# Performance work log

Hardware: AMD Instinct MI355X
Metric: run time of the kernel (lower is better)

Reference implementation:

```python
import jax, jax.numpy as jnp
import numpy as np
from jax import lax

B, S, D, H_HEADS, K, G, E, HID = 2, 1024, 1024, 16, 31, 4, 2, 2048
HD = D // H_HEADS

def _layer_norm(x, g, b, eps=1e-5):
    mu = jnp.mean(x, axis=-1, keepdims=True)
    var = jnp.mean(jnp.square(x - mu), axis=-1, keepdims=True)
    return (x - mu) * lax.rsqrt(var + eps) * g + b

def setup_inputs() -> dict:
    key = jax.random.key(0)
    ks = jax.random.split(key, 16)
    s = 0.02
    return {
        "x": jax.random.normal(ks[0], (B, S, D), jnp.float32),
        "group_ids": jax.random.randint(ks[1], (B, S), 0, G, jnp.int32),
        "cn_g": jnp.ones((D,), jnp.float32), "cn_b": jnp.zeros((D,), jnp.float32),
        "conv_w": jax.random.normal(ks[2], (D, D, K), jnp.float32) * s,
        "conv_b": jnp.zeros((D,), jnp.float32),
        "an_g": jnp.ones((D,), jnp.float32), "an_b": jnp.zeros((D,), jnp.float32),
        "in_w": jax.random.normal(ks[3], (3 * D, D), jnp.float32) * s,
        "in_b": jnp.zeros((3 * D,), jnp.float32),
        "out_w": jax.random.normal(ks[4], (D, D), jnp.float32) * s,
        "out_b": jnp.zeros((D,), jnp.float32),
        "e_w1": jax.random.normal(ks[5], (G, E, D, HID), jnp.float32) * s,
        "e_b1": jnp.zeros((G, E, HID), jnp.float32),
        "e_w2": jax.random.normal(ks[6], (G, E, HID, D), jnp.float32) * s,
        "e_b2": jnp.zeros((G, E, D), jnp.float32),
    }

def reference(x, group_ids, cn_g, cn_b, conv_w, conv_b, an_g, an_b,
              in_w, in_b, out_w, out_b, e_w1, e_b1, e_w2, e_b2):
    # ---- conv block (dropout off: deterministic/eval) ----
    residual = x
    h = _layer_norm(x, cn_g, cn_b)
    hc = jnp.transpose(h, (0, 2, 1))  # [B, D, S]
    hc = lax.conv_general_dilated(hc, conv_w, window_strides=(1,),
                                  padding=[(K // 2, K // 2)],
                                  dimension_numbers=("NCH", "OIH", "NCH"))
    hc = hc + conv_b[None, :, None]
    hc = jnp.transpose(hc, (0, 2, 1))
    x = jax.nn.gelu(hc, approximate=False) + residual
    # ---- self-attention block ----
    residual = x
    h = _layer_norm(x, an_g, an_b)
    qkv = h @ in_w.T + in_b  # [B, S, 3D]
    q, k, v = jnp.split(qkv, 3, axis=-1)
    q = q.reshape(B, S, H_HEADS, HD)
    k = k.reshape(B, S, H_HEADS, HD)
    v = v.reshape(B, S, H_HEADS, HD)
    scores = jnp.einsum("bqhd,bkhd->bhqk", q, k) / jnp.sqrt(jnp.float32(HD))
    attn = jax.nn.softmax(scores, axis=-1)
    ctx = jnp.einsum("bhqk,bkhd->bqhd", attn, v).reshape(B, S, D)
    x = ctx @ out_w.T + out_b + residual
    # ---- group-routed MoE (dense compute over groups, select by group id) ----
    residual = x
    xf = x.reshape(B * S, D)
    gid = group_ids.reshape(B * S)
    h1 = jax.nn.gelu(jnp.einsum("nd,gedh->ngeh", xf, e_w1) + e_b1, approximate=False)
    out_all = jnp.einsum("ngeh,gehd->nged", h1, e_w2) + e_b2  # [N, G, E, D]
    out_all = jnp.mean(out_all, axis=2)  # mean over experts in group -> [N, G, D]
    sel = jnp.take_along_axis(out_all, gid[:, None, None].astype(jnp.int32), axis=1)[:, 0]
    x = sel.reshape(B, S, D) + residual
    return x
```

## Files before the change

kernel.cpp:

```cpp
#include <hip/hip_runtime.h>
#include <hip/hip_bf16.h>
#include <math.h>

#define BB 2
#define SS 1024
#define DD 1024
#define HH 16
#define HDIM 64
#define KK 31
#define GG 4
#define EE 2
#define HIDN 2048
#define NTOK (BB*SS)
#define D3 (3*DD)

typedef unsigned short u16;
typedef __attribute__((ext_vector_type(8))) short s16x8;
typedef __attribute__((ext_vector_type(8))) unsigned short u16x8;
typedef __attribute__((ext_vector_type(4))) unsigned short u16x4;
typedef __attribute__((ext_vector_type(2))) unsigned short u16x2;
typedef __attribute__((ext_vector_type(4))) float f32x4;
typedef __attribute__((ext_vector_type(2))) unsigned int u32x2;

__device__ __forceinline__ float gelu_f(float x) {
  return 0.5f * x * (1.0f + erff(x * 0.7071067811865475f));
}
__device__ __forceinline__ u16 f2bf(float f) {
  unsigned u = __builtin_bit_cast(unsigned, f);
  u = (u + 0x7fffu + ((u >> 16) & 1u)) >> 16;
  return (u16)u;
}
__device__ __forceinline__ float bf2f(u16 u) {
  return __builtin_bit_cast(float, ((unsigned)u) << 16);
}
__device__ __forceinline__ f32x4 MFMA16(s16x8 a, s16x8 b, f32x4 c) {
  return __builtin_amdgcn_mfma_f32_16x16x32_bf16(a, b, c, 0, 0, 0);
}
#define GLOAD16(gp, lp) __builtin_amdgcn_global_load_lds( \
    (const __attribute__((address_space(1))) void*)(gp),  \
    (__attribute__((address_space(3))) void*)(lp), 16, 0, 0)

__global__ void ln_kernel(const float* __restrict__ x, const float* __restrict__ g,
                          const float* __restrict__ b, u16* __restrict__ out) {
  const int row = blockIdx.x;
  const int tid = threadIdx.x;
  __shared__ float red[4];
  const float4 v = reinterpret_cast<const float4*>(x + (size_t)row * DD)[tid];
  float s = v.x + v.y + v.z + v.w;
  s += __shfl_down(s, 32); s += __shfl_down(s, 16); s += __shfl_down(s, 8);
  s += __shfl_down(s, 4);  s += __shfl_down(s, 2);  s += __shfl_down(s, 1);
  if ((tid & 63) == 0) red[tid >> 6] = s;
  __syncthreads();
  const float mean = (red[0] + red[1] + red[2] + red[3]) * (1.0f / DD);
  __syncthreads();
  const float4 d = make_float4(v.x - mean, v.y - mean, v.z - mean, v.w - mean);
  float sq = d.x*d.x + d.y*d.y + d.z*d.z + d.w*d.w;
  sq += __shfl_down(sq, 32); sq += __shfl_down(sq, 16); sq += __shfl_down(sq, 8);
  sq += __shfl_down(sq, 4);  sq += __shfl_down(sq, 2);  sq += __shfl_down(sq, 1);
  if ((tid & 63) == 0) red[tid >> 6] = sq;
  __syncthreads();
  const float var = (red[0] + red[1] + red[2] + red[3]) * (1.0f / DD);
  const float rstd = rsqrtf(var + 1e-5f);
  const float4 gv = reinterpret_cast<const float4*>(g)[tid];
  const float4 bv = reinterpret_cast<const float4*>(b)[tid];
  u16x4 o;
  o[0] = f2bf(d.x * rstd * gv.x + bv.x);
  o[1] = f2bf(d.y * rstd * gv.y + bv.y);
  o[2] = f2bf(d.z * rstd * gv.z + bv.z);
  o[3] = f2bf(d.w * rstd * gv.w + bv.w);
  *reinterpret_cast<u16x4*>(out + (size_t)row * DD + tid * 4) = o;
}

__global__ void prep_convw(const float* __restrict__ cw, u16* __restrict__ Wb) {
  const int o = blockIdx.x;
  const int i4 = threadIdx.x * 4;
  float wv[4][KK];
#pragma unroll
  for (int j = 0; j < 4; ++j) {
    const float* src = cw + ((size_t)o * DD + i4 + j) * KK;
#pragma unroll
    for (int k = 0; k < KK; ++k) wv[j][k] = src[k];
  }
#pragma unroll
  for (int k = 0; k < KK; ++k) {
    u16x4 o4;
    o4[0] = f2bf(wv[0][k]); o4[1] = f2bf(wv[1][k]);
    o4[2] = f2bf(wv[2][k]); o4[3] = f2bf(wv[3][k]);
    *(u16x4*)&Wb[((size_t)k * DD + o) * DD + i4] = o4;
  }
}

__global__ void cvt_kernel(const float* __restrict__ in, u16* __restrict__ outp, int n4) {
  const int i = blockIdx.x * 256 + threadIdx.x;
  if (i < n4) {
    const float4 v = reinterpret_cast<const float4*>(in)[i];
    u16x4 o; o[0] = f2bf(v.x); o[1] = f2bf(v.y); o[2] = f2bf(v.z); o[3] = f2bf(v.w);
    reinterpret_cast<u16x4*>(outp)[i] = o;
  }
}

__global__ void tr_kernel(const float* __restrict__ src, u16* __restrict__ dst, int R, int C) {
  __shared__ float tile[32][33];
  const int c0 = blockIdx.x * 32, r0 = blockIdx.y * 32;
  const size_t base = (size_t)blockIdx.z * R * C;
  const int tx = threadIdx.x & 31, ty = threadIdx.x >> 5;
#pragma unroll
  for (int i = 0; i < 4; ++i)
    tile[ty + i * 8][tx] = src[base + (size_t)(r0 + ty + i * 8) * C + c0 + tx];
  __syncthreads();
  const int rx = threadIdx.x & 15, cy = threadIdx.x >> 4;
#pragma unroll
  for (int i = 0; i < 2; ++i) {
    const int c = cy + i * 16;
    u16x2 o2;
    o2[0] = f2bf(tile[2 * rx][c]);
    o2[1] = f2bf(tile[2 * rx + 1][c]);
    *(u16x2*)&dst[base + (size_t)(c0 + c) * R + r0 + 2 * rx] = o2;
  }
}

__global__ __launch_bounds__(512) void conv_kernel(const u16* __restrict__ hb,
                                                   const u16* __restrict__ Wb,
                                                   u16* __restrict__ P) {
  const int L = blockIdx.x;
  const int o_t = L & 7;
  const int rest = L >> 3;
  const int s_t = rest >> 1;
  const int z = rest & 1;
  const int b = s_t >> 3, sloc = s_t & 7;
  const int s0l = sloc * 128;
  const int o0 = o_t * 128;
  const int ibase = z * 512;
  const int tid = threadIdx.x, lane = tid & 63, w = tid >> 6;
  const int wm = (w >> 2) & 1, wn = (w >> 1) & 1, ksid = w & 1;
  const int q15 = lane & 15, g = lane >> 4;
  __shared__ __align__(16) u16 Ad[2][160 * 64];
  __shared__ __align__(16) u16 Bp[8][3][2048];
  const int rlo = (sloc == 0) ? 15 : 0;
  const int rhi = (sloc == 7) ? 143 : 158;
  if (sloc == 0)
    for (int i = tid; i < 15 * 64; i += 512) { Ad[0][i] = 0; Ad[1][i] = 0; }
  if (sloc == 7)
    for (int i = tid; i < 17 * 64; i += 512) { Ad[0][143 * 64 + i] = 0; Ad[1][143 * 64 + i] = 0; }
  auto stageA = [&](int buf, int i0) {
    for (int q = w; q < 20; q += 8) {
      const int r = q * 8 + (lane >> 3);
      const int c = (lane & 7) ^ (r & 7);
      if (r >= rlo && r < rhi)
        GLOAD16(hb + (size_t)(b * SS + s0l - 15 + r) * DD + i0 + c * 8, &Ad[buf][q * 512]);
    }
  };
  auto stageBp = [&](int slot, int k, int i0w) {
#pragma unroll
    for (int q = 0; q < 4; ++q) {
      const int j = lane >> 2;
      const int r = q * 16 + j;
      const int c16 = (lane & 3) ^ ((j >> 1) & 3);
      GLOAD16(Wb + ((size_t)k * DD + o0 + wn * 64 + r) * DD + i0w + c16 * 8,
              &Bp[w][slot][q * 512]);
    }
  };
  f32x4 acc[4][4];
#pragma unroll
  for (int i = 0; i < 4; ++i)
#pragma unroll
    for (int j = 0; j < 4; ++j) acc[i][j] = f32x4{0.f, 0.f, 0.f, 0.f};
  const int ib0 = ibase + ksid * 32;
  stageA(0, ibase);
  stageBp(0, 0, ib0);
  stageBp(1, 1, ib0);
  asm volatile("s_waitcnt vmcnt(0)" ::: "memory");
  __syncthreads();
  const int T = 8 * KK;
  const int kx = ksid * 64;
  const int bro = q15 * 64 + ((g ^ ((q15 >> 1) & 3)) << 4);
  int t = 0;
  for (int i0i = 0; i0i < 8; ++i0i) {
    const u16* Ab = Ad[i0i & 1];
    for (int k = 0; k < KK; ++k, ++t) {
      {
        const int tn = t + 2;
        if (tn < T) stageBp(tn % 3, tn % KK, ibase + (tn / KK) * 64 + ksid * 32);
      }
      s16x8 af[4];
      const int rk0 = wm * 64 + q15 + k;
#pragma unroll
      for (int mf = 0; mf < 4; ++mf) {
        const int rr = rk0 + mf * 16;
        const char* p = (const char*)Ab + rr * 128;
        af[mf] = *(const s16x8*)(p + (((g ^ (rr & 7)) * 16) ^ kx));
      }
      if (t + 2 < T)      asm volatile("s_waitcnt vmcnt(8)" ::: "memory");
      else if (t + 1 < T) asm volatile("s_waitcnt vmcnt(4)" ::: "memory");
      else                asm volatile("s_waitcnt vmcnt(0)" ::: "memory");
      if (k == 5 && i0i < 7) stageA((i0i + 1) & 1, ibase + (i0i + 1) * 64);
      const char* Bb = (const char*)&Bp[w][t % 3][0];
      s16x8 bfr[4];
#pragma unroll
      for (int nf = 0; nf < 4; ++nf)
        bfr[nf] = *(const s16x8*)(Bb + nf * 1024 + bro);
      __builtin_amdgcn_s_setprio(1);
#pragma unroll
      for (int mf = 0; mf < 4; ++mf)
#pragma unroll
        for (int nf = 0; nf < 4; ++nf)
          acc[mf][nf] = MFMA16(af[mf], bfr[nf], acc[mf][nf]);
      __builtin_amdgcn_s_setprio(0);
    }
    if (i0i < 7) {
      asm volatile("s_waitcnt vmcnt(0)" ::: "memory");
      __syncthreads();
    }
  }
  __syncthreads();
  float* scr = (float*)(&Bp[0][0][0]) + (wm * 2 + wn) * 4096;
  if (ksid == 1) {
#pragma unroll
    for (int mf = 0; mf < 4; ++mf)
#pragma unroll
      for (int nf = 0; nf < 4; ++nf) {
        const int col = nf * 16 + q15;
        *(f32x4*)&scr[col * 64 + ((mf * 16 + g * 4) ^ ((col & 7) << 3))] = acc[mf][nf];
      }
  }
  __syncthreads();
  if (ksid == 0) {
    u16* Pz = P + (size_t)z * NTOK * DD;
#pragma unroll
    for (int mf = 0; mf < 4; ++mf) {
      f32x4 sum[4];
#pragma unroll
      for (int nf = 0; nf < 4; ++nf) {
        const int col = nf * 16 + q15;
        const f32x4 o = *(const f32x4*)&scr[col * 64 + ((mf * 16 + g * 4) ^ ((col & 7) << 3))];
        sum[nf] = acc[mf][nf] + o;
      }
#pragma unroll
      for (int r = 0; r < 4; ++r) {
        const int srow = s0l + wm * 64 + mf * 16 + g * 4 + r;
        u16* orow = Pz + (size_t)(b * SS + srow) * DD + o0 + wn * 64;
#pragma unroll
        for (int nf = 0; nf < 4; ++nf)
          orow[nf * 16 + q15] = f2bf(sum[nf][r]);
      }
    }
  }
}

__global__ void combine_kernel(const u16* __restrict__ P, const float* __restrict__ cb,
                               const float* __restrict__ x, const float* __restrict__ an_g,
                               const float* __restrict__ an_b, float* __restrict__ x1,
                               u16* __restrict__ hb) {
  const int row = blockIdx.x;
  const int tid = threadIdx.x;
  const size_t base = (size_t)row * DD + tid * 4;
  const int col = tid * 4;
  __shared__ float red[4];
  const u16x4 p0 = *(const u16x4*)(P + base);
  const u16x4 p1 = *(const u16x4*)(P + (size_t)NTOK * DD + base);
  const float4 xv = *(const float4*)(x + base);
  const float4 cbv = *(const float4*)(cb + col);
  float4 v;
  v.x = gelu_f(bf2f(p0[0]) + bf2f(p1[0]) + cbv.x) + xv.x;
  v.y = gelu_f(bf2f(p0[1]) + bf2f(p1[1]) + cbv.y) + xv.y;
  v.z = gelu_f(bf2f(p0[2]) + bf2f(p1[2]) + cbv.z) + xv.z;
  v.w = gelu_f(bf2f(p0[3]) + bf2f(p1[3]) + cbv.w) + xv.w;
  *(float4*)(x1 + base) = v;
  float s = v.x + v.y + v.z + v.w;
  s += __shfl_down(s, 32); s += __shfl_down(s, 16); s += __shfl_down(s, 8);
  s += __shfl_down(s, 4);  s += __shfl_down(s, 2);  s += __shfl_down(s, 1);
  if ((tid & 63) == 0) red[tid >> 6] = s;
  __syncthreads();
  const float mean = (red[0] + red[1] + red[2] + red[3]) * (1.0f / DD);
  __syncthreads();
  const float4 d = make_float4(v.x - mean, v.y - mean, v.z - mean, v.w - mean);
  float sq = d.x*d.x + d.y*d.y + d.z*d.z + d.w*d.w;
  sq += __shfl_down(sq, 32); sq += __shfl_down(sq, 16); sq += __shfl_down(sq, 8);
  sq += __shfl_down(sq, 4);  sq += __shfl_down(sq, 2);  sq += __shfl_down(sq, 1);
  if ((tid & 63) == 0) red[tid >> 6] = sq;
  __syncthreads();
  const float var = (red[0] + red[1] + red[2] + red[3]) * (1.0f / DD);
  const float rstd = rsqrtf(var + 1e-5f);
  const float4 gv = reinterpret_cast<const float4*>(an_g)[tid];
  const float4 bv = reinterpret_cast<const float4*>(an_b)[tid];
  u16x4 o;
  o[0] = f2bf(d.x * rstd * gv.x + bv.x);
  o[1] = f2bf(d.y * rstd * gv.y + bv.y);
  o[2] = f2bf(d.z * rstd * gv.z + bv.z);
  o[3] = f2bf(d.w * rstd * gv.w + bv.w);
  *reinterpret_cast<u16x4*>(hb + (size_t)row * DD + tid * 4) = o;
}

__global__ __launch_bounds__(256) void qkv_kernel(const u16* __restrict__ A, const u16* __restrict__ B,
                           const float* __restrict__ bias, u16* __restrict__ C,
                           u16* __restrict__ Vt) {
  const int n0 = blockIdx.x * 128, m0 = blockIdx.y * 128;
  const int tid = threadIdx.x, lane = tid & 63, w = tid >> 6;
  const int wm = w >> 1, wn = w & 1;
  __shared__ __align__(16) u16 As[2][128 * 64];
  __shared__ __align__(16) u16 Bs[2][128 * 64];
  f32x4 acc[4][4];
#pragma unroll
  for (int i = 0; i < 4; ++i)
#pragma unroll
    for (int j = 0; j < 4; ++j) acc[i][j] = f32x4{0.f, 0.f, 0.f, 0.f};
  auto stage = [&](int t, int buf) {
    const int k0 = t * 64;
#pragma unroll
    for (int q = 0; q < 4; ++q) {
      const int idx = w * 4 + q, r = idx * 8 + (lane >> 3), c = (lane & 7) ^ (r & 7);
      GLOAD16(A + (size_t)(m0 + r) * DD + k0 + c * 8, &As[buf][idx * 512]);
    }
#pragma unroll
    for (int q = 0; q < 4; ++q) {
      const int idx = w * 4 + q, r = idx * 8 + (lane >> 3), c = (lane & 7) ^ (r & 7);
      GLOAD16(B + (size_t)(n0 + r) * DD + k0 + c * 8, &Bs[buf][idx * 512]);
    }
  };
  stage(0, 0);
  asm volatile("s_waitcnt vmcnt(0)" ::: "memory");
  __syncthreads();
  const int T = DD / 64;
  for (int t = 0; t < T; ++t) {
    if (t > 0) {
      asm volatile("s_waitcnt vmcnt(0)" ::: "memory");
      __builtin_amdgcn_s_barrier();
      asm volatile("" ::: "memory");
    }
    if (t + 1 < T) stage(t + 1, (t + 1) & 1);
    const u16* Ab = As[t & 1];
    const u16* Bb = Bs[t & 1];
    const int xb = (((lane >> 4) ^ (lane & 7)) * 16);
    s16x8 af[4][2], bfr[4][2];
#pragma unroll
    for (int mf = 0; mf < 4; ++mf) {
      const char* p = (const char*)Ab + (wm * 64 + mf * 16 + (lane & 15)) * 128;
      af[mf][0] = *(const s16x8*)(p + xb);
      af[mf][1] = *(const s16x8*)(p + (xb ^ 64));
    }
#pragma unroll
    for (int nf = 0; nf < 4; ++nf) {
      const char* p = (const char*)Bb + (wn * 64 + nf * 16 + (lane & 15)) * 128;
      bfr[nf][0] = *(const s16x8*)(p + xb);
      bfr[nf][1] = *(const s16x8*)(p + (xb ^ 64));
    }
    __builtin_amdgcn_s_setprio(1);
#pragma unroll
    for (int ks = 0; ks < 2; ++ks)
#pragma unroll
      for (int mf = 0; mf < 4; ++mf)
#pragma unroll
        for (int nf = 0; nf < 4; ++nf)
          acc[mf][nf] = MFMA16(af[mf][ks], bfr[nf][ks], acc[mf][nf]);
    __builtin_amdgcn_s_setprio(0);
  }
  if (n0 < 2 * DD) {
#pragma unroll
    for (int mf = 0; mf < 4; ++mf)
#pragma unroll
      for (int rr = 0; rr < 4; ++rr) {
        const int row = m0 + wm * 64 + mf * 16 + (lane >> 4) * 4 + rr;
#pragma unroll
        for (int nf = 0; nf < 4; ++nf) {
          const int col = n0 + wn * 64 + nf * 16 + (lane & 15);
          C[(size_t)row * D3 + col] = f2bf(acc[mf][nf][rr] + bias[col]);
        }
      }
  } else {
    u16* tbuf = (u16*)&As[0][0];
    __syncthreads();
#pragma unroll
    for (int mf = 0; mf < 4; ++mf)
#pragma unroll
      for (int rr = 0; rr < 4; ++rr) {
        const int row = wm * 64 + mf * 16 + (lane >> 4) * 4 + rr;
#pragma unroll
        for (int nf = 0; nf < 4; ++nf) {
          const int col = wn * 64 + nf * 16 + (lane & 15);
          tbuf[col * 128 + row] = f2bf(acc[mf][nf][rr] + bias[n0 + col]);
        }
      }
    __syncthreads();
    const int b = m0 >> 10, s0 = m0 & 1023;
    const int cv0 = n0 - 2 * DD;
    const int rowl = tid >> 1, half = tid & 1;
    const int cv = cv0 + rowl;
    const int h = cv >> 6, dch = cv & 63;
    const u16* srcp = tbuf + rowl * 128 + half * 64;
    u16* dstp = Vt + ((size_t)(b * HH + h) * HDIM + dch) * SS + s0 + half * 64;
#pragma unroll
    for (int i = 0; i < 8; ++i)
      *(u16x8*)(dstp + i * 8) = *(const u16x8*)(srcp + i * 8);
  }
}

__global__ __launch_bounds__(256) void out_kernel(const u16* __restrict__ A, const u16* __restrict__ B,
                           const float* __restrict__ bias, const float* __restrict__ resid,
                           float* __restrict__ C, u16* __restrict__ x2g,
                           const int* __restrict__ inv) {
  const int n0 = blockIdx.x * 64, m0 = blockIdx.y * 128;
  const int tid = threadIdx.x, lane = tid & 63, w = tid >> 6;
  const int wm = w >> 1, wn = w & 1;
  __shared__ u16 As[3][128 * 64];
  __shared__ u16 Bs[3][64 * 64];
  f32x4 acc[4][2];
#pragma unroll
  for (int i = 0; i < 4; ++i)
#pragma unroll
    for (int j = 0; j < 2; ++j) acc[i][j] = f32x4{0.f, 0.f, 0.f, 0.f};
  auto stage = [&](int t, int buf) {
    const int k0 = t * 64;
#pragma unroll
    for (int q = 0; q < 4; ++q) {
      const int idx = w * 4 + q, r = idx * 8 + (lane >> 3), c = (lane & 7) ^ (r & 7);
      GLOAD16(A + (size_t)(m0 + r) * DD + k0 + c * 8, &As[buf][idx * 512]);
    }
#pragma unroll
    for (int q = 0; q < 2; ++q) {
      const int idx = w * 2 + q, r = idx * 8 + (lane >> 3), c = (lane & 7) ^ (r & 7);
      GLOAD16(B + (size_t)(n0 + r) * DD + k0 + c * 8, &Bs[buf][idx * 512]);
    }
  };
  stage(0, 0);
  stage(1, 1);
  const int T = DD / 64;
  for (int t = 0; t < T; ++t) {
    if (t + 1 < T) asm volatile("s_waitcnt vmcnt(6)" ::: "memory");
    else           asm volatile("s_waitcnt vmcnt(0)" ::: "memory");
    __builtin_amdgcn_s_barrier();
    asm volatile("" ::: "memory");
    if (t + 2 < T) stage(t + 2, (t + 2) % 3);
    const u16* Ab = As[t % 3];
    const u16* Bb = Bs[t % 3];
    const int xb = (((lane >> 4) ^ (lane & 7)) * 16);
    s16x8 af[4][2], bfr[2][2];
#pragma unroll
    for (int mf = 0; mf < 4; ++mf) {
      const char* p = (const char*)Ab + (wm * 64 + mf * 16 + (lane & 15)) * 128;
      af[mf][0] = *(const s16x8*)(p + xb);
      af[mf][1] = *(const s16x8*)(p + (xb ^ 64));
    }
#pragma unroll
    for (int nf = 0; nf < 2; ++nf) {
      const char* p = (const char*)Bb + (wn * 32 + nf * 16 + (lane & 15)) * 128;
      bfr[nf][0] = *(const s16x8*)(p + xb);
      bfr[nf][1] = *(const s16x8*)(p + (xb ^ 64));
    }
    __builtin_amdgcn_s_setprio(1);
#pragma unroll
    for (int ks = 0; ks < 2; ++ks)
#pragma unroll
      for (int mf = 0; mf < 4; ++mf)
#pragma unroll
        for (int nf = 0; nf < 2; ++nf)
          acc[mf][nf] = MFMA16(af[mf][ks], bfr[nf][ks], acc[mf][nf]);
    __builtin_amdgcn_s_setprio(0);
  }
#pragma unroll
  for (int mf = 0; mf < 4; ++mf)
#pragma unroll
    for (int rr = 0; rr < 4; ++rr) {
      const int row = m0 + wm * 64 + mf * 16 + (lane >> 4) * 4 + rr;
      const int slot = inv[row];
#pragma unroll
      for (int nf = 0; nf < 2; ++nf) {
        const int col = n0 + wn * 32 + nf * 16 + (lane & 15);
        const float v = acc[mf][nf][rr] + bias[col] + resid[(size_t)row * DD + col];
        C[(size_t)row * DD + col] = v;
        x2g[(size_t)slot * DD + col] = f2bf(v);
      }
    }
}

__global__ __launch_bounds__(512) void attn_kernel(const u16* __restrict__ qkv,
                                                   const u16* __restrict__ Vt,
                                                   u16* __restrict__ ctx) {
  const int q0 = blockIdx.x * 128, h = blockIdx.y, b = blockIdx.z;
  const int tid = threadIdx.x, lane = tid & 63, w = tid >> 6;
  const int q15 = lane & 15, g = lane >> 4, l7 = lane & 7;
  __shared__ u16 Q_lds[128 * 64];
  __shared__ u16 K_lds[2][64 * 64];
  __shared__ u16 V_lds[2][64 * 64];
  __shared__ u16 P_lds[8][16 * 72];
  __shared__ float s_lds[8][16];

#pragma unroll
  for (int q2 = 0; q2 < 2; ++q2) {
    const int idx = w * 2 + q2;
    const int r = idx * 8 + (lane >> 3);
    const int c = l7 ^ (r & 7);
    GLOAD16(qkv + (size_t)(b * SS + q0 + r) * D3 + h * HDIM + c * 8, &Q_lds[idx * 512]);
  }
  auto stageK = [&](int buf, int kt) {
    const int r = w * 8 + (lane >> 3);
    const int c = l7 ^ (r & 7);
    GLOAD16(qkv + (size_t)(b * SS + kt * 64 + r) * D3 + DD + h * HDIM + c * 8,
            &K_lds[buf][w * 512]);
  };
  auto stageV = [&](int buf, int kt) {
    const int r = w * 8 + (lane >> 3);
    const int c = l7 ^ (r & 7);
    GLOAD16(Vt + ((size_t)(b * HH + h) * HDIM + r) * SS + kt * 64 + c * 8,
            &V_lds[buf][w * 512]);
  };
  stageK(0, 0);
  stageV(0, 0);
  asm volatile("s_waitcnt vmcnt(0)" ::: "memory");
  __syncthreads();
  s16x8 bq[2];
#pragma unroll
  for (int ks = 0; ks < 2; ++ks)
    bq[ks] = *(const s16x8*)((const char*)Q_lds + (w * 16 + q15) * 128 + ((4 * ks + g) ^ l7) * 16);
  f32x4 oacc[4];
#pragma unroll
  for (int nf = 0; nf < 4; ++nf) oacc[nf] = f32x4{0.f, 0.f, 0.f, 0.f};
  float mrun = -3.0e38f, lrun = 0.0f;
  int buf = 0;
  for (int kt = 0; kt < 16; ++kt) {
    if (kt < 15) { stageK(buf ^ 1, kt + 1); stageV(buf ^ 1, kt + 1); }
    f32x4 st[4];
#pragma unroll
    for (int mf = 0; mf < 4; ++mf) st[mf] = f32x4{0.f, 0.f, 0.f, 0.f};
#pragma unroll
    for (int ks = 0; ks < 2; ++ks) {
#pragma unroll
      for (int mf = 0; mf < 4; ++mf) {
        const s16x8 ka = *(const s16x8*)((const char*)K_lds[buf] + (mf * 16 + q15) * 128 +
                                         ((4 * ks + g) ^ l7) * 16);
        st[mf] = MFMA16(ka, bq[ks], st[mf]);
      }
    }
    float t0[4][4];
    float cmax = -3.0e38f;
#pragma unroll
    for (int mf = 0; mf < 4; ++mf)
#pragma unroll
      for (int r = 0; r < 4; ++r) {
        const float v = st[mf][r] * 0.125f;
        t0[mf][r] = v;
        cmax = fmaxf(cmax, v);
      }
    cmax = fmaxf(cmax, __shfl_xor(cmax, 16));
    cmax = fmaxf(cmax, __shfl_xor(cmax, 32));
    const float mnew = fmaxf(mrun, cmax);
    const float scf = __expf(mrun - mnew);
    float psum = 0.f;
#pragma unroll
    for (int mf = 0; mf < 4; ++mf)
#pragma unroll
      for (int r = 0; r < 4; ++r) {
        const float p = __expf(t0[mf][r] - mnew);
        t0[mf][r] = p;
        psum += p;
      }
    psum += __shfl_xor(psum, 16);
    psum += __shfl_xor(psum, 32);
    lrun = lrun * scf + psum;
    mrun = mnew;
    s_lds[w][q15] = scf;
    u16* pw = &P_lds[w][0];
#pragma unroll
    for (int mf = 0; mf < 4; ++mf) {
      u32x2 pk;
      pk[0] = (unsigned)f2bf(t0[mf][0]) | ((unsigned)f2bf(t0[mf][1]) << 16);
      pk[1] = (unsigned)f2bf(t0[mf][2]) | ((unsigned)f2bf(t0[mf][3]) << 16);
      *(u32x2*)(pw + q15 * 72 + mf * 16 + g * 4) = pk;
    }
    asm volatile("s_waitcnt lgkmcnt(0)" ::: "memory");
    const f32x4 scv = *(const f32x4*)&s_lds[w][g * 4];
#pragma unroll
    for (int nf = 0; nf < 4; ++nf)
#pragma unroll
      for (int r = 0; r < 4; ++r) oacc[nf][r] *= scv[r];
#pragma unroll
    for (int ks = 0; ks < 2; ++ks) {
      const s16x8 pa = *(const s16x8*)(pw + q15 * 72 + ks * 32 + g * 8);
#pragma unroll
      for (int nf = 0; nf < 4; ++nf) {
        const s16x8 bv = *(const s16x8*)((const char*)V_lds[buf] + (nf * 16 + q15) * 128 +
                                         ((4 * ks + g) ^ l7) * 16);
        oacc[nf] = MFMA16(pa, bv, oacc[nf]);
      }
    }
    asm volatile("s_waitcnt vmcnt(0)" ::: "memory");
    __syncthreads();
    buf ^= 1;
  }
  const float linv = 1.0f / lrun;
  s_lds[w][q15] = linv;
  asm volatile("s_waitcnt lgkmcnt(0)" ::: "memory");
  const f32x4 lv = *(const f32x4*)&s_lds[w][g * 4];
#pragma unroll
  for (int nf = 0; nf < 4; ++nf)
#pragma unroll
    for (int r = 0; r < 4; ++r) {
      const int qg = q0 + w * 16 + g * 4 + r;
      ctx[(size_t)(b * SS + qg) * DD + h * HDIM + nf * 16 + q15] = f2bf(oacc[nf][r] * lv[r]);
    }
}

__global__ void routing_kernel(const int* __restrict__ gid, int* __restrict__ cnts_g,
                               int* __restrict__ off_g, int* __restrict__ gidx,
                               int* __restrict__ inv) {
  __shared__ int cnt[GG];
  __shared__ int off[GG + 1];
  const int tid = threadIdx.x;
  if (tid < GG) cnt[tid] = 0;
  __syncthreads();
  const int t0 = tid, t1 = tid + 1024;
  const int g0 = gid[t0], g1 = gid[t1];
  const int s0 = atomicAdd(&cnt[g0], 1);
  const int s1 = atomicAdd(&cnt[g1], 1);
  __syncthreads();
  if (tid == 0) {
    int s = 0;
#pragma unroll
    for (int g = 0; g < GG; ++g) { off[g] = s; s += cnt[g]; }
    off[GG] = s;
  }
  __syncthreads();
  const int sg0 = off[g0] + s0;
  gidx[sg0] = t0; inv[t0] = sg0;
  const int sg1 = off[g1] + s1;
  gidx[sg1] = t1; inv[t1] = sg1;
  if (tid < GG) cnts_g[tid] = cnt[tid];
  if (tid <= GG) off_g[tid] = off[tid];
}

__global__ __launch_bounds__(256) void moe1_kernel(const u16* __restrict__ x2g, const u16* __restrict__ w1t,
                            const float* __restrict__ e_b1, const int* __restrict__ off,
                            const int* __restrict__ cnts, u16* __restrict__ h1) {
  const int ge = blockIdx.z, g = ge >> 1, e = ge & 1;
  const int cnt = cnts[g];
  const int m0 = blockIdx.y * 128;
  if (m0 >= cnt) return;
  const int base = off[g];
  const int n0 = blockIdx.x * 128;
  const u16* A = x2g + (size_t)base * DD;
  const u16* B = w1t + (size_t)ge * HIDN * DD;
  const int tid = threadIdx.x, lane = tid & 63, w = tid >> 6;
  const int wm = w >> 1, wn = w & 1;
  __shared__ u16 As[2][128 * 64];
  __shared__ u16 Bs[2][128 * 64];
  f32x4 acc[4][4];
#pragma unroll
  for (int i = 0; i < 4; ++i)
#pragma unroll
    for (int j = 0; j < 4; ++j) acc[i][j] = f32x4{0.f, 0.f, 0.f, 0.f};
  auto stage = [&](int t, int buf) {
    const int k0 = t * 64;
#pragma unroll
    for (int q = 0; q < 4; ++q) {
      const int idx = w * 4 + q, r = idx * 8 + (lane >> 3), c = (lane & 7) ^ (r & 7);
      int rg = m0 + r; if (rg > cnt - 1) rg = cnt - 1;
      GLOAD16(A + (size_t)rg * DD + k0 + c * 8, &As[buf][idx * 512]);
    }
#pragma unroll
    for (int q = 0; q < 4; ++q) {
      const int idx = w * 4 + q, r = idx * 8 + (lane >> 3), c = (lane & 7) ^ (r & 7);
      GLOAD16(B + (size_t)(n0 + r) * DD + k0 + c * 8, &Bs[buf][idx * 512]);
    }
  };
  stage(0, 0);
  asm volatile("s_waitcnt vmcnt(0)" ::: "memory");
  __syncthreads();
  const int T = DD / 64;
  for (int t = 0; t < T; ++t) {
    if (t > 0) {
      asm volatile("s_waitcnt vmcnt(0)" ::: "memory");
      __builtin_amdgcn_s_barrier();
      asm volatile("" ::: "memory");
    }
    if (t + 1 < T) stage(t + 1, (t + 1) & 1);
    const u16* Ab = As[t & 1];
    const u16* Bb = Bs[t & 1];
    const int xb = (((lane >> 4) ^ (lane & 7)) * 16);
    s16x8 af[4][2], bfr[4][2];
#pragma unroll
    for (int mf = 0; mf < 4; ++mf) {
      const char* p = (const char*)Ab + (wm * 64 + mf * 16 + (lane & 15)) * 128;
      af[mf][0] = *(const s16x8*)(p + xb);
      af[mf][1] = *(const s16x8*)(p + (xb ^ 64));
    }
#pragma unroll
    for (int nf = 0; nf < 4; ++nf) {
      const char* p = (const char*)Bb + (wn * 64 + nf * 16 + (lane & 15)) * 128;
      bfr[nf][0] = *(const s16x8*)(p + xb);
      bfr[nf][1] = *(const s16x8*)(p + (xb ^ 64));
    }
    __builtin_amdgcn_s_setprio(1);
#pragma unroll
    for (int ks = 0; ks < 2; ++ks)
#pragma unroll
      for (int mf = 0; mf < 4; ++mf)
#pragma unroll
        for (int nf = 0; nf < 4; ++nf)
          acc[mf][nf] = MFMA16(af[mf][ks], bfr[nf][ks], acc[mf][nf]);
    __builtin_amdgcn_s_setprio(0);
  }
  const float* b1 = e_b1 + (size_t)ge * HIDN;
#pragma unroll
  for (int mf = 0; mf < 4; ++mf)
#pragma unroll
    for (int rr = 0; rr < 4; ++rr) {
      const int rowg = m0 + wm * 64 + mf * 16 + (lane >> 4) * 4 + rr;
      if (rowg < cnt) {
        u16* orow = h1 + ((size_t)e * NTOK + base + rowg) * HIDN;
#pragma unroll
        for (int nf = 0; nf < 4; ++nf) {
          const int col = n0 + wn * 64 + nf * 16 + (lane & 15);
          orow[col] = f2bf(gelu_f(acc[mf][nf][rr] + b1[col]));
        }
      }
    }
}

__global__ __launch_bounds__(512) void moe2_kernel(const u16* __restrict__ h1, const u16* __restrict__ w2t,
                            const float* __restrict__ e_b2, const int* __restrict__ off,
                            const int* __restrict__ cnts, const int* __restrict__ gidx,
                            const float* __restrict__ x2, float* __restrict__ outp) {
  const int g = blockIdx.z;
  const int cnt = cnts[g];
  const int m0 = blockIdx.y * 128;
  if (m0 >= cnt) return;
  const int base = off[g];
  const int n0 = blockIdx.x * 64;
  const int tid = threadIdx.x, lane = tid & 63, w = tid >> 6;
  const int wm = (w >> 2) & 1, wn = (w >> 1) & 1, ksid = w & 1;
  const int q15 = lane & 15, gq = lane >> 4;
  __shared__ __align__(16) u16 As[3][128 * 64];
  __shared__ __align__(16) u16 Bs[3][64 * 64];
  f32x4 acc[4][2];
#pragma unroll
  for (int i = 0; i < 4; ++i)
#pragma unroll
    for (int j = 0; j < 2; ++j) acc[i][j] = f32x4{0.f, 0.f, 0.f, 0.f};
  auto stage = [&](int t, int buf) {
    const int e = t >> 5;
    const int k0 = (t & 31) * 64;
#pragma unroll
    for (int q = 0; q < 2; ++q) {
      const int idx = w * 2 + q, r = idx * 8 + (lane >> 3), c = (lane & 7) ^ (r & 7);
      int rg = m0 + r; if (rg > cnt - 1) rg = cnt - 1;
      GLOAD16(h1 + ((size_t)e * NTOK + base + rg) * HIDN + k0 + c * 8, &As[buf][idx * 512]);
    }
    {
      const int r = w * 8 + (lane >> 3), c = (lane & 7) ^ (r & 7);
      GLOAD16(w2t + ((size_t)(g * EE + e) * DD + n0 + r) * HIDN + k0 + c * 8, &Bs[buf][w * 512]);
    }
  };
  stage(0, 0);
  stage(1, 1);
  const int T = 64;
  const int kx = ksid * 64;
  for (int t = 0; t < T; ++t) {
    if (t + 1 < T) asm volatile("s_waitcnt vmcnt(3)" ::: "memory");
    else           asm volatile("s_waitcnt vmcnt(0)" ::: "memory");
    __builtin_amdgcn_s_barrier();
    asm volatile("" ::: "memory");
    if (t + 2 < T) stage(t + 2, (t + 2) % 3);
    const u16* Ab = As[t % 3];
    const u16* Bb = Bs[t % 3];
    const int xb = ((((lane >> 4) ^ (lane & 7)) * 16) ^ kx);
    s16x8 af[4], bfr[2];
#pragma unroll
    for (int mf = 0; mf < 4; ++mf) {
      const char* p = (const char*)Ab + (wm * 64 + mf * 16 + q15) * 128;
      af[mf] = *(const s16x8*)(p + xb);
    }
#pragma unroll
    for (int nf = 0; nf < 2; ++nf) {
      const char* p = (const char*)Bb + (wn * 32 + nf * 16 + q15) * 128;
      bfr[nf] = *(const s16x8*)(p + xb);
    }
    __builtin_amdgcn_s_setprio(1);
#pragma unroll
    for (int mf = 0; mf < 4; ++mf)
#pragma unroll
      for (int nf = 0; nf < 2; ++nf)
        acc[mf][nf] = MFMA16(af[mf], bfr[nf], acc[mf][nf]);
    __builtin_amdgcn_s_setprio(0);
  }
  __syncthreads();
  float* scr = (float*)&As[0][0] + (wm * 2 + wn) * 2048;
  if (ksid == 1) {
#pragma unroll
    for (int mf = 0; mf < 4; ++mf)
#pragma unroll
      for (int nf = 0; nf < 2; ++nf) {
        const int col = nf * 16 + q15;
        *(f32x4*)&scr[col * 64 + ((mf * 16 + gq * 4) ^ ((col & 7) << 3))] = acc[mf][nf];
      }
  }
  __syncthreads();
  if (ksid == 0) {
    const float* b20 = e_b2 + (size_t)(g * EE + 0) * DD;
    const float* b21 = e_b2 + (size_t)(g * EE + 1) * DD;
#pragma unroll
    for (int mf = 0; mf < 4; ++mf) {
      f32x4 sum[2];
#pragma unroll
      for (int nf = 0; nf < 2; ++nf) {
        const int col = nf * 16 + q15;
        const f32x4 o = *(const f32x4*)&scr[col * 64 + ((mf * 16 + gq * 4) ^ ((col & 7) << 3))];
        sum[nf] = acc[mf][nf] + o;
      }
#pragma unroll
      for (int rr = 0; rr < 4; ++rr) {
        const int rowg = m0 + wm * 64 + mf * 16 + gq * 4 + rr;
        if (rowg < cnt) {
          const int tok = gidx[base + rowg];
#pragma unroll
          for (int nf = 0; nf < 2; ++nf) {
            const int col = n0 + wn * 32 + nf * 16 + q15;
            outp[(size_t)tok * DD + col] =
                0.5f * sum[nf][rr] + 0.5f * (b20[col] + b21[col]) + x2[(size_t)tok * DD + col];
          }
        }
      }
    }
  }
}

extern "C" void kernel_launch(void* const* d_in, const int* in_sizes, int n_in,
                              void* d_out, int out_size, void* d_ws, size_t ws_size,
                              hipStream_t stream) {
  (void)in_sizes; (void)n_in; (void)out_size; (void)ws_size;
  const float* x      = (const float*)d_in[0];
  const int*   gid    = (const int*)d_in[1];
  const float* cn_g   = (const float*)d_in[2];
  const float* cn_b   = (const float*)d_in[3];
  const float* conv_w = (const float*)d_in[4];
  const float* conv_b = (const float*)d_in[5];
  const float* an_g   = (const float*)d_in[6];
  const float* an_b   = (const float*)d_in[7];
  const float* in_w   = (const float*)d_in[8];
  const float* in_b   = (const float*)d_in[9];
  const float* out_w  = (const float*)d_in[10];
  const float* out_b  = (const float*)d_in[11];
  const float* e_w1   = (const float*)d_in[12];
  const float* e_b1   = (const float*)d_in[13];
  const float* e_w2   = (const float*)d_in[14];
  const float* e_b2   = (const float*)d_in[15];
  float* outp = (float*)d_out;

  char* wsp = (char*)d_ws;
  u16*   hb    = (u16*)(wsp);
  u16*   Pc    = (u16*)(wsp + (4ull << 20));
  float* x1    = (float*)(wsp + (12ull << 20));
  u16*   Wb    = (u16*)(wsp + (12ull << 20));
  u16*   qkvb  = (u16*)(wsp + (24ull << 20));
  u16*   inwb  = (u16*)(wsp + (40ull << 20));
  u16*   outwb = (u16*)(wsp + (40ull << 20));
  u16*   Vt    = (u16*)(wsp + (46ull << 20));
  u16*   ctxb  = hb;
  float* x2    = (float*)(wsp + (52ull << 20));
  int*   inv   = (int*)(wsp + (60ull << 20));
  u16*   x2g   = (u16*)(wsp + (64ull << 20));
  u16*   wgt   = (u16*)(wsp + (4ull << 20));
  u16*   h1    = (u16*)(wsp + (36ull << 20));
  int*   gat   = (int*)(wsp + (74ull << 20));
  int*   cnts  = gat + GG * NTOK;
  int*   offp  = cnts + GG;
  int*   gidx  = offp + (GG + 1);

  ln_kernel<<<NTOK, 256, 0, stream>>>(x, cn_g, cn_b, hb);
  prep_convw<<<1024, 256, 0, stream>>>(conv_w, Wb);
  conv_kernel<<<256, 512, 0, stream>>>(hb, Wb, Pc);
  combine_kernel<<<NTOK, 256, 0, stream>>>(Pc, conv_b, x, an_g, an_b, x1, hb);
  routing_kernel<<<1, 1024, 0, stream>>>(gid, cnts, offp, gidx, inv);
  cvt_kernel<<<3072, 256, 0, stream>>>(in_w, inwb, 3 * DD * DD / 4);
  qkv_kernel<<<dim3(D3 / 128, NTOK / 128), 256, 0, stream>>>(hb, inwb, in_b, qkvb, Vt);
  attn_kernel<<<dim3(SS / 128, HH, BB), 512, 0, stream>>>(qkvb, Vt, ctxb);
  cvt_kernel<<<1024, 256, 0, stream>>>(out_w, outwb, DD * DD / 4);
  out_kernel<<<dim3(DD / 64, NTOK / 128), 256, 0, stream>>>(ctxb, outwb, out_b, x1, x2, x2g, inv);
  tr_kernel<<<dim3(HIDN / 32, DD / 32, GG * EE), 256, 0, stream>>>(e_w1, wgt, DD, HIDN);
  moe1_kernel<<<dim3(HIDN / 128, NTOK / 128, GG * EE), 256, 0, stream>>>(x2g, wgt, e_b1, offp, cnts, h1);
  tr_kernel<<<dim3(DD / 32, HIDN / 32, GG * EE), 256, 0, stream>>>(e_w2, wgt, HIDN, DD);
  moe2_kernel<<<dim3(DD / 64, NTOK / 128, GG), 512, 0, stream>>>(h1, wgt, e_b2, offp, cnts, gidx, x2, outp);
}
```

Measured before the change: 466.1 us.

## Split conv input channels four ways with shared B tiles and fp32 partials

The conv kernel now splits the input-channel reduction into four slices instead of two, launching 512 blocks instead of 256. Weight tiles are staged once per block into a shared triple buffer instead of per-warp copies, and A staging drops double buffering to cut LDS use so more blocks fit per CU. Partials are written as fp32 and summed across four slices in the combine kernel. This raises parallelism and occupancy but doubles partial-sum memory traffic, adds per-step barriers, and serializes A restaging between slices.

```diff
diff --git a/kernel.cpp b/kernel.cpp
--- a/kernel.cpp
+++ b/kernel.cpp
@@ -119,45 +119,44 @@
   }
 }
 
-__global__ __launch_bounds__(512) void conv_kernel(const u16* __restrict__ hb,
-                                                   const u16* __restrict__ Wb,
-                                                   u16* __restrict__ P) {
+__global__ __launch_bounds__(512, 4) void conv_kernel(const u16* __restrict__ hb,
+                                                      const u16* __restrict__ Wb,
+                                                      float* __restrict__ P) {
   const int L = blockIdx.x;
   const int o_t = L & 7;
   const int rest = L >> 3;
-  const int s_t = rest >> 1;
-  const int z = rest & 1;
+  const int s_t = rest >> 2;
+  const int z = rest & 3;
   const int b = s_t >> 3, sloc = s_t & 7;
   const int s0l = sloc * 128;
   const int o0 = o_t * 128;
-  const int ibase = z * 512;
+  const int ibase = z * 256;
   const int tid = threadIdx.x, lane = tid & 63, w = tid >> 6;
   const int wm = (w >> 2) & 1, wn = (w >> 1) & 1, ksid = w & 1;
   const int q15 = lane & 15, g = lane >> 4;
-  __shared__ __align__(16) u16 Ad[2][160 * 64];
-  __shared__ __align__(16) u16 Bp[8][3][2048];
+  __shared__ __align__(16) u16 Ad[160 * 64];
+  __shared__ __align__(16) u16 Bs[3][128 * 64];
   const int rlo = (sloc == 0) ? 15 : 0;
   const int rhi = (sloc == 7) ? 143 : 158;
   if (sloc == 0)
-    for (int i = tid; i < 15 * 64; i += 512) { Ad[0][i] = 0; Ad[1][i] = 0; }
+    for (int i = tid; i < 15 * 64; i += 512) Ad[i] = 0;
   if (sloc == 7)
-    for (int i = tid; i < 17 * 64; i += 512) { Ad[0][143 * 64 + i] = 0; Ad[1][143 * 64 + i] = 0; }
-  auto stageA = [&](int buf, int i0) {
+    for (int i = tid; i < 17 * 64; i += 512) Ad[143 * 64 + i] = 0;
+  auto stageA = [&](int i0) {
     for (int q = w; q < 20; q += 8) {
       const int r = q * 8 + (lane >> 3);
       const int c = (lane & 7) ^ (r & 7);
       if (r >= rlo && r < rhi)
-        GLOAD16(hb + (size_t)(b * SS + s0l - 15 + r) * DD + i0 + c * 8, &Ad[buf][q * 512]);
+        GLOAD16(hb + (size_t)(b * SS + s0l - 15 + r) * DD + i0 + c * 8, &Ad[q * 512]);
     }
   };
-  auto stageBp = [&](int slot, int k, int i0w) {
-#pragma unroll
-    for (int q = 0; q < 4; ++q) {
-      const int j = lane >> 2;
-      const int r = q * 16 + j;
-      const int c16 = (lane & 3) ^ ((j >> 1) & 3);
-      GLOAD16(Wb + ((size_t)k * DD + o0 + wn * 64 + r) * DD + i0w + c16 * 8,
-              &Bp[w][slot][q * 512]);
+  auto stageB = [&](int slot, int k, int i0) {
+#pragma unroll
+    for (int qq = 0; qq < 2; ++qq) {
+      const int q = w * 2 + qq;
+      const int r = q * 8 + (lane >> 3);
+      const int c = (lane & 7) ^ (r & 7);
+      GLOAD16(Wb + ((size_t)k * DD + o0 + r) * DD + i0 + c * 8, &Bs[slot][q * 512]);
     }
   };
   f32x4 acc[4][4];
@@ -165,40 +164,41 @@
   for (int i = 0; i < 4; ++i)
 #pragma unroll
     for (int j = 0; j < 4; ++j) acc[i][j] = f32x4{0.f, 0.f, 0.f, 0.f};
-  const int ib0 = ibase + ksid * 32;
-  stageA(0, ibase);
-  stageBp(0, 0, ib0);
-  stageBp(1, 1, ib0);
+  stageA(ibase);
+  stageB(0, 0, ibase);
+  stageB(1, 1, ibase);
   asm volatile("s_waitcnt vmcnt(0)" ::: "memory");
   __syncthreads();
-  const int T = 8 * KK;
+  const int NSL = 4;
+  const int T = NSL * KK;
   const int kx = ksid * 64;
-  const int bro = q15 * 64 + ((g ^ ((q15 >> 1) & 3)) << 4);
   int t = 0;
-  for (int i0i = 0; i0i < 8; ++i0i) {
-    const u16* Ab = Ad[i0i & 1];
+  for (int i0i = 0; i0i < NSL; ++i0i) {
     for (int k = 0; k < KK; ++k, ++t) {
+      if (t + 1 < T) asm volatile("s_waitcnt vmcnt(2)" ::: "memory");
+      else           asm volatile("s_waitcnt vmcnt(0)" ::: "memory");
+      __builtin_amdgcn_s_barrier();
+      asm volatile("" ::: "memory");
       {
         const int tn = t + 2;
-        if (tn < T) stageBp(tn % 3, tn % KK, ibase + (tn / KK) * 64 + ksid * 32);
+        if (tn < T) stageB(tn % 3, tn % KK, ibase + (tn / KK) * 64);
       }
       s16x8 af[4];
       const int rk0 = wm * 64 + q15 + k;
 #pragma unroll
       for (int mf = 0; mf < 4; ++mf) {
         const int rr = rk0 + mf * 16;
-        const char* p = (const char*)Ab + rr * 128;
+        const char* p = (const char*)Ad + rr * 128;
         af[mf] = *(const s16x8*)(p + (((g ^ (rr & 7)) * 16) ^ kx));
       }
-      if (t + 2 < T)      asm volatile("s_waitcnt vmcnt(8)" ::: "memory");
-      else if (t + 1 < T) asm volatile("s_waitcnt vmcnt(4)" ::: "memory");
-      else                asm volatile("s_waitcnt vmcnt(0)" ::: "memory");
-      if (k == 5 && i0i < 7) stageA((i0i + 1) & 1, ibase + (i0i + 1) * 64);
-      const char* Bb = (const char*)&Bp[w][t % 3][0];
+      const u16* Bb = Bs[t % 3];
       s16x8 bfr[4];
 #pragma unroll
-      for (int nf = 0; nf < 4; ++nf)
-        bfr[nf] = *(const s16x8*)(Bb + nf * 1024 + bro);
+      for (int nf = 0; nf < 4; ++nf) {
+        const int rr = wn * 64 + nf * 16 + q15;
+        const char* p = (const char*)Bb + rr * 128;
+        bfr[nf] = *(const s16x8*)(p + (((g ^ (rr & 7)) * 16) ^ kx));
+      }
       __builtin_amdgcn_s_setprio(1);
 #pragma unroll
       for (int mf = 0; mf < 4; ++mf)
@@ -207,13 +207,17 @@
           acc[mf][nf] = MFMA16(af[mf], bfr[nf], acc[mf][nf]);
       __builtin_amdgcn_s_setprio(0);
     }
-    if (i0i < 7) {
+    if (i0i < NSL - 1) {
       asm volatile("s_waitcnt vmcnt(0)" ::: "memory");
       __syncthreads();
-    }
-  }
-  __syncthreads();
-  float* scr = (float*)(&Bp[0][0][0]) + (wm * 2 + wn) * 4096;
+      stageA(ibase + (i0i + 1) * 64);
+      asm volatile("s_waitcnt vmcnt(0)" ::: "memory");
+      __syncthreads();
+    }
+  }
+  __syncthreads();
+  const int pair = wm * 2 + wn;
+  float* scr = (pair < 3) ? ((float*)&Bs[pair][0]) : (float*)&Ad[0];
   if (ksid == 1) {
 #pragma unroll
     for (int mf = 0; mf < 4; ++mf)
@@ -225,7 +229,7 @@
   }
   __syncthreads();
   if (ksid == 0) {
-    u16* Pz = P + (size_t)z * NTOK * DD;
+    float* Pz = P + (size_t)z * NTOK * DD;
 #pragma unroll
     for (int mf = 0; mf < 4; ++mf) {
       f32x4 sum[4];
@@ -238,16 +242,16 @@
 #pragma unroll
       for (int r = 0; r < 4; ++r) {
         const int srow = s0l + wm * 64 + mf * 16 + g * 4 + r;
-        u16* orow = Pz + (size_t)(b * SS + srow) * DD + o0 + wn * 64;
+        float* orow = Pz + (size_t)(b * SS + srow) * DD + o0 + wn * 64;
 #pragma unroll
         for (int nf = 0; nf < 4; ++nf)
-          orow[nf * 16 + q15] = f2bf(sum[nf][r]);
-      }
-    }
-  }
-}
-
-__global__ void combine_kernel(const u16* __restrict__ P, const float* __restrict__ cb,
+          orow[nf * 16 + q15] = sum[nf][r];
+      }
+    }
+  }
+}
+
+__global__ void combine_kernel(const float* __restrict__ P, const float* __restrict__ cb,
                                const float* __restrict__ x, const float* __restrict__ an_g,
                                const float* __restrict__ an_b, float* __restrict__ x1,
                                u16* __restrict__ hb) {
@@ -256,15 +260,19 @@
   const size_t base = (size_t)row * DD + tid * 4;
   const int col = tid * 4;
   __shared__ float red[4];
-  const u16x4 p0 = *(const u16x4*)(P + base);
-  const u16x4 p1 = *(const u16x4*)(P + (size_t)NTOK * DD + base);
+  float4 p = *(const float4*)(P + base);
+#pragma unroll
+  for (int zz = 1; zz < 4; ++zz) {
+    const float4 q = *(const float4*)(P + (size_t)zz * NTOK * DD + base);
+    p.x += q.x; p.y += q.y; p.z += q.z; p.w += q.w;
+  }
   const float4 xv = *(const float4*)(x + base);
   const float4 cbv = *(const float4*)(cb + col);
   float4 v;
-  v.x = gelu_f(bf2f(p0[0]) + bf2f(p1[0]) + cbv.x) + xv.x;
-  v.y = gelu_f(bf2f(p0[1]) + bf2f(p1[1]) + cbv.y) + xv.y;
-  v.z = gelu_f(bf2f(p0[2]) + bf2f(p1[2]) + cbv.z) + xv.z;
-  v.w = gelu_f(bf2f(p0[3]) + bf2f(p1[3]) + cbv.w) + xv.w;
+  v.x = gelu_f(p.x + cbv.x) + xv.x;
+  v.y = gelu_f(p.y + cbv.y) + xv.y;
+  v.z = gelu_f(p.z + cbv.z) + xv.z;
+  v.w = gelu_f(p.w + cbv.w) + xv.w;
   *(float4*)(x1 + base) = v;
   float s = v.x + v.y + v.z + v.w;
   s += __shfl_down(s, 32); s += __shfl_down(s, 16); s += __shfl_down(s, 8);
@@ -846,16 +854,16 @@
 
   char* wsp = (char*)d_ws;
   u16*   hb    = (u16*)(wsp);
-  u16*   Pc    = (u16*)(wsp + (4ull << 20));
-  float* x1    = (float*)(wsp + (12ull << 20));
-  u16*   Wb    = (u16*)(wsp + (12ull << 20));
+  float* Pc    = (float*)(wsp + (4ull << 20));
+  u16*   Wb    = (u16*)(wsp + (36ull << 20));
+  float* x1    = (float*)(wsp + (36ull << 20));
   u16*   qkvb  = (u16*)(wsp + (24ull << 20));
-  u16*   inwb  = (u16*)(wsp + (40ull << 20));
-  u16*   outwb = (u16*)(wsp + (40ull << 20));
-  u16*   Vt    = (u16*)(wsp + (46ull << 20));
+  u16*   inwb  = (u16*)(wsp + (44ull << 20));
+  u16*   outwb = (u16*)(wsp + (44ull << 20));
+  u16*   Vt    = (u16*)(wsp + (50ull << 20));
   u16*   ctxb  = hb;
-  float* x2    = (float*)(wsp + (52ull << 20));
-  int*   inv   = (int*)(wsp + (60ull << 20));
+  float* x2    = (float*)(wsp + (54ull << 20));
+  int*   inv   = (int*)(wsp + (62ull << 20));
   u16*   x2g   = (u16*)(wsp + (64ull << 20));
   u16*   wgt   = (u16*)(wsp + (4ull << 20));
   u16*   h1    = (u16*)(wsp + (36ull << 20));
@@ -866,7 +874,7 @@
 
   ln_kernel<<<NTOK, 256, 0, stream>>>(x, cn_g, cn_b, hb);
   prep_convw<<<1024, 256, 0, stream>>>(conv_w, Wb);
-  conv_kernel<<<256, 512, 0, stream>>>(hb, Wb, Pc);
+  conv_kernel<<<512, 512, 0, stream>>>(hb, Wb, Pc);
   combine_kernel<<<NTOK, 256, 0, stream>>>(Pc, conv_b, x, an_g, an_b, x1, hb);
   routing_kernel<<<1, 1024, 0, stream>>>(gid, cnts, offp, gidx, inv);
   cvt_kernel<<<3072, 256, 0, stream>>>(in_w, inwb, 3 * DD * DD / 4);
```

Result: faster. 410.4 us, median of 2 (-11.9%).
